# Performance work log

Hardware: AMD Instinct MI355X
Metric: run time of the kernel (lower is better)

The kernel has to match this reference:

```python
import jax, jax.numpy as jnp
import numpy as np

B, S, D = 2, 2048, 768
H, HD = 12, 64
PAST = 2048
MAXPOS = PAST + S  # 4096


def setup_inputs() -> dict:
    key = jax.random.key(0)
    ks = jax.random.split(key, 9)
    hidden_states = jax.random.normal(ks[0], (B, S, D), dtype=jnp.float32)
    layer_past = jax.random.normal(ks[1], (2, B, H, PAST, HD), dtype=jnp.float32)
    # GPT-2 style causal multiplicative mask over full context length
    mask = jnp.tril(jnp.ones((MAXPOS, MAXPOS), dtype=jnp.float32))[None, None, :, :]
    Wq = jax.random.normal(ks[2], (D, D), dtype=jnp.float32) * 0.02
    bq = jnp.zeros((D,), dtype=jnp.float32)
    Wk = jax.random.normal(ks[3], (D, D), dtype=jnp.float32) * 0.02
    bk = jnp.zeros((D,), dtype=jnp.float32)
    Wv = jax.random.normal(ks[4], (D, D), dtype=jnp.float32) * 0.02
    bv = jnp.zeros((D,), dtype=jnp.float32)
    return {"hidden_states": hidden_states, "layer_past": layer_past, "mask": mask,
            "Wq": Wq, "bq": bq, "Wk": Wk, "bk": bk, "Wv": Wv, "bv": bv}


def _split_heads(x):
    b, s, _ = x.shape
    return x.reshape(b, s, H, HD).transpose(0, 2, 1, 3)  # [B,H,S,HD]


def reference(hidden_states, layer_past, mask, Wq, bq, Wk, bk, Wv, bv):
    q = _split_heads(hidden_states @ Wq + bq)
    k = _split_heads(hidden_states @ Wk + bk)
    v = _split_heads(hidden_states @ Wv + bv)
    # KV-cache concat along sequence dim
    k = jnp.concatenate((layer_past[0], k), axis=-2)  # [B,H,ns,HD]
    v = jnp.concatenate((layer_past[1], v), axis=-2)
    present = jnp.stack((k, v), axis=0)
    scores = jnp.einsum('bhqd,bhkd->bhqk', q, k) / 8.0  # 8 = sqrt(64)
    nd, ns = scores.shape[-2], scores.shape[-1]
    m = mask[:, :, ns - nd:ns, :ns]
    scores = scores * m - 1e10 * (1.0 - m)
    probs = jax.nn.softmax(scores, axis=-1)  # dropout is identity at eval
    ctx = jnp.einsum('bhqk,bhkd->bhqd', probs, v)
    ctx = ctx.transpose(0, 2, 1, 3).reshape(hidden_states.shape[0], nd, H * HD)
    return ctx, present
```

## Files before the change

### kernel.cpp

```cpp
#include <hip/hip_runtime.h>


typedef unsigned short u16;
typedef __attribute__((ext_vector_type(8))) short bf16x8;
typedef __attribute__((ext_vector_type(4))) float f32x4;

#define CTXN   3145728
#define CHUNK  262144
#define PCHUNK 131072
#define SHAD_NEED ((size_t)12*1024*1024 + (size_t)2*24*64*4096*2)
#define MFMA(a,b,c) __builtin_amdgcn_mfma_f32_16x16x32_bf16(a,b,c,0,0,0)

__device__ __forceinline__ u16 f2b(float f) {
    union { float f; unsigned int i; } u; u.f = f;
    unsigned int r = u.i + 0x7fffu + ((u.i >> 16) & 1u);
    return (u16)(r >> 16);
}
__device__ __forceinline__ unsigned int pk2(float lo, float hi) {
    unsigned int lr = __float_as_uint(lo); lr += 0x7fffu + ((lr >> 16) & 1u);
    unsigned int hr = __float_as_uint(hi); hr += 0x7fffu + ((hr >> 16) & 1u);
    return __builtin_amdgcn_perm(hr, lr, 0x07060302u);
}
union U8 { unsigned int w[4]; bf16x8 v; };

__device__ __forceinline__ int vpos(int k) {
    return (k & 32) | ((k & 12) << 1) | ((k & 16) >> 2) | (k & 3);
}
__device__ __forceinline__ int vkey(int p) {
    return (p & 32) | ((p & 4) << 2) | ((p & 24) >> 1) | (p & 3);
}

__global__ __launch_bounds__(256) void prep_w(
    const float* __restrict__ Wq, const float* __restrict__ Wk,
    const float* __restrict__ Wv, u16* __restrict__ WT)
{
    __shared__ __align__(16) u16 tile[64][72];
    const float* W = blockIdx.z == 0 ? Wq : (blockIdx.z == 1 ? Wk : Wv);
    const int r0 = blockIdx.y * 64, c0 = blockIdx.x * 64;
    const int t = threadIdx.x;
#pragma unroll
    for (int i = 0; i < 2; i++) {
        int idx = t + 256 * i, r = idx >> 3, c8 = idx & 7;
        const float* src = &W[(size_t)(r0 + r) * 768 + c0 + c8 * 8];
        u16 tmp[8];
#pragma unroll
        for (int j = 0; j < 8; j++) tmp[j] = f2b(src[j]);
        *(uint4*)&tile[r][c8 * 8] = *(uint4*)tmp;
    }
    __syncthreads();
#pragma unroll
    for (int i = 0; i < 2; i++) {
        int idx = t + 256 * i, n = idx >> 3, k8 = idx & 7;
        u16 tmp[8];
#pragma unroll
        for (int j = 0; j < 8; j++) tmp[j] = tile[k8 * 8 + j][n];
        *(uint4*)&WT[((size_t)blockIdx.z * 768 + c0 + n) * 768 + r0 + k8 * 8] = *(uint4*)tmp;
    }
}

__global__ __launch_bounds__(256) void prep_h(const float* __restrict__ Hs,
                                              u16* __restrict__ Hb)
{
    size_t base = ((size_t)blockIdx.x * 256 + threadIdx.x) * 16;
    u16 tmp[16];
#pragma unroll
    for (int j = 0; j < 16; j++) tmp[j] = f2b(Hs[base + j]);
    *(uint4*)&Hb[base] = *(uint4*)tmp;
    *(uint4*)&Hb[base + 8] = *(uint4*)(tmp + 8);
}

__global__ __launch_bounds__(256) void past_prep(const float* __restrict__ past,
                                                 float* __restrict__ out,
                                                 u16* __restrict__ shad)
{
    __shared__ float Vl[64][65];
    const int bh = blockIdx.x, kb = blockIdx.y, t = threadIdx.x;
    const int key = t >> 2, qd = t & 3;
    const float* Ks = past + (size_t)bh * PCHUNK + (size_t)kb * 4096;
    const float* Vs = past + (size_t)(24 + bh) * PCHUNK + (size_t)kb * 4096;
    float* Ko = out + (size_t)CTXN + (size_t)bh * CHUNK + (size_t)kb * 4096;
    float* Vo = out + (size_t)CTXN + (size_t)(24 + bh) * CHUNK + (size_t)kb * 4096;

    float4 kv[4], vv[4];
#pragma unroll
    for (int j = 0; j < 4; j++) {
        kv[j] = *(const float4*)&Ks[key * 64 + qd * 16 + j * 4];
        vv[j] = *(const float4*)&Vs[key * 64 + qd * 16 + j * 4];
    }
#pragma unroll
    for (int j = 0; j < 4; j++) {
        *(float4*)&Ko[key * 64 + qd * 16 + j * 4] = kv[j];
        *(float4*)&Vo[key * 64 + qd * 16 + j * 4] = vv[j];
        *(float4*)&Vl[key][qd * 16 + j * 4] = vv[j];
    }
    if (shad) {
        u16* Ksh = shad + (size_t)(bh * 64 + kb) * 4096;
        const float* kf = (const float*)kv;
        u16 a[8], bb[8];
#pragma unroll
        for (int j = 0; j < 8; j++) { a[j] = f2b(kf[j]); bb[j] = f2b(kf[8 + j]); }
        *(uint4*)&Ksh[key * 64 + (((2 * qd) ^ (key & 7)) * 8)] = *(uint4*)a;
        *(uint4*)&Ksh[key * 64 + (((2 * qd + 1) ^ (key & 7)) * 8)] = *(uint4*)bb;
    }
    __syncthreads();
    if (shad) {
        u16* Vsh = shad + (size_t)(1536 + bh * 64 + kb) * 4096;
        const int d = t & 63, ph = t >> 6;
#pragma unroll
        for (int s2 = 0; s2 < 2; s2++) {
            int sp = ph * 2 + s2;
            u16 c[8];
#pragma unroll
            for (int j = 0; j < 8; j++)
                c[j] = f2b(Vl[vkey(sp * 8 + j)][d]);
            *(uint4*)&Vsh[d * 64 + ((sp ^ (d & 7)) * 8)] = *(uint4*)c;
        }
    }
}

__global__ __launch_bounds__(256) void qkv_gemm(
    const u16* __restrict__ Hb, const u16* __restrict__ WT,
    const float* __restrict__ bq, const float* __restrict__ bk,
    const float* __restrict__ bv, float* out, u16* shad)
{
    __shared__ __align__(16) u16 Al[128][72];
    __shared__ __align__(16) u16 Bl[128][72];
    const int t = threadIdx.x, lane = t & 63, w = t >> 6;
    const int wr = w >> 1, wc = w & 1;
    const int g = lane >> 4, li = lane & 15;
    const int m0 = blockIdx.y * 128, n0 = blockIdx.x * 128;
    f32x4 acc[4][4] = {};

    for (int k0 = 0; k0 < 768; k0 += 64) {
#pragma unroll
        for (int i = 0; i < 4; i++) {
            int idx = t + 256 * i, r = idx >> 3, c8 = idx & 7;
            *(uint4*)&Al[r][c8 * 8] = *(const uint4*)&Hb[(size_t)(m0 + r) * 768 + k0 + c8 * 8];
            *(uint4*)&Bl[r][c8 * 8] = *(const uint4*)&WT[(size_t)(n0 + r) * 768 + k0 + c8 * 8];
        }
        __syncthreads();
#pragma unroll
        for (int kk = 0; kk < 64; kk += 32) {
            bf16x8 af[4], bf[4];
#pragma unroll
            for (int mi = 0; mi < 4; mi++)
                af[mi] = *(const bf16x8*)&Al[wr * 64 + mi * 16 + li][kk + g * 8];
#pragma unroll
            for (int ni = 0; ni < 4; ni++)
                bf[ni] = *(const bf16x8*)&Bl[wc * 64 + ni * 16 + li][kk + g * 8];
#pragma unroll
            for (int mi = 0; mi < 4; mi++)
#pragma unroll
                for (int ni = 0; ni < 4; ni++)
                    acc[mi][ni] = MFMA(af[mi], bf[ni], acc[mi][ni]);
        }
        __syncthreads();
    }

#pragma unroll
    for (int mi = 0; mi < 4; mi++) {
#pragma unroll
        for (int ni = 0; ni < 4; ni++) {
            int col = n0 + wc * 64 + ni * 16 + li;
            int which = col >= 1536 ? 2 : (col >= 768 ? 1 : 0);
            int c2 = col - which * 768;
            int h = c2 >> 6, hd = c2 & 63;
            float bias = which == 0 ? bq[c2] : which == 1 ? bk[c2] : bv[c2];
            int rowb = m0 + wr * 64 + mi * 16 + g * 4;
#pragma unroll
            for (int r = 0; r < 4; r++) {
                int rr = rowb + r;
                float o = acc[mi][ni][r] + bias;
                if (which == 0) {
                    out[(size_t)rr * 768 + c2] = o;
                } else {
                    int b = rr >> 11, s = rr & 2047;
                    size_t off = (size_t)CTXN +
                        ((size_t)((which - 1) * 2 + b) * 12 + h) * CHUNK +
                        (size_t)(2048 + s) * 64 + hd;
                    out[off] = o;
                    if (shad) {
                        int bh2 = b * 12 + h;
                        int keyg = 2048 + s;
                        u16 ob = f2b(o);
                        if (which == 1)
                            shad[((size_t)(bh2 * 64 + (keyg >> 6))) * 4096
                                 + (keyg & 63) * 64 + (((hd >> 3) ^ (keyg & 7)) * 8)
                                 + (hd & 7)] = ob;
                        else {
                            int pos = vpos(keyg & 63);
                            shad[((size_t)(1536 + bh2 * 64 + (keyg >> 6))) * 4096
                                 + hd * 64 + (((pos >> 3) ^ (hd & 7)) * 8)
                                 + (pos & 7)] = ob;
                        }
                    }
                }
            }
        }
    }
}

#define SOFTMAX_RESCALE(S, M, L, O)                                              \
    {                                                                            \
        float tm = fmaxf(fmaxf(S[0][0], S[0][1]), fmaxf(S[0][2], S[0][3]));      \
        _Pragma("unroll")                                                        \
        for (int nt = 1; nt < 8; nt++)                                           \
            tm = fmaxf(tm, fmaxf(fmaxf(S[nt][0], S[nt][1]),                      \
                                 fmaxf(S[nt][2], S[nt][3])));                    \
        tm = fmaxf(tm, __shfl_xor(tm, 16));                                      \
        tm = fmaxf(tm, __shfl_xor(tm, 32));                                      \
        float mn = fmaxf(M, tm);                                                 \
        float al = __builtin_amdgcn_exp2f(M - mn);                               \
        M = mn;                                                                  \
        float ts = 0.f;                                                          \
        _Pragma("unroll")                                                        \
        for (int nt = 0; nt < 8; nt++) {                                         \
            _Pragma("unroll")                                                    \
            for (int r = 0; r < 4; r++) {                                        \
                float p = __builtin_amdgcn_exp2f(S[nt][r] - mn);                 \
                S[nt][r] = p; ts += p;                                           \
            }                                                                    \
        }                                                                        \
        ts += __shfl_xor(ts, 16);                                                \
        ts += __shfl_xor(ts, 32);                                                \
        L = L * al + ts;                                                         \
        float av[4];                                                             \
        _Pragma("unroll")                                                        \
        for (int r = 0; r < 4; r++) av[r] = __shfl(al, (g << 4) + (g << 2) + r); \
        _Pragma("unroll")                                                        \
        for (int dt = 0; dt < 4; dt++) {                                         \
            _Pragma("unroll")                                                    \
            for (int r = 0; r < 4; r++) O[dt][r] *= av[r];                       \
        }                                                                        \
    }

__global__ __launch_bounds__(128, 2) void attn2(const u16* __restrict__ shad, float* out)
{
    __shared__ __align__(16) u16 KV[16384];
    const int bh = blockIdx.x;
    const int qt = 31 - blockIdx.y;
    const int b = bh / 12, h = bh - 12 * b;
    const int t = threadIdx.x, lane = t & 63, w = t >> 6;
    const int g = lane >> 4, li = lane & 15, liq = li & 7;
    char* ldsb = (char*)KV;
    const char* Kp = (const char*)(shad + (size_t)bh * 262144);
    const char* Vp = (const char*)(shad + (size_t)(1536 + bh * 64) * 4096);

    const int qw = qt * 64 + w * 32;
    const float qs = 0.125f * 1.44269504f;
    u16 qa[32];
    const float* QA = out + ((size_t)b * 2048 + qw + li) * 768 + h * 64;
    const float* QB = QA + 16 * 768;
#pragma unroll
    for (int j = 0; j < 8; j++) {
        qa[j]      = f2b(QA[g * 8 + j] * qs);
        qa[8 + j]  = f2b(QA[32 + g * 8 + j] * qs);
        qa[16 + j] = f2b(QB[g * 8 + j] * qs);
        qa[24 + j] = f2b(QB[32 + g * 8 + j] * qs);
    }
    bf16x8 qA0 = *(bf16x8*)qa,        qA1 = *(bf16x8*)(qa + 8);
    bf16x8 qB0 = *(bf16x8*)(qa + 16), qB1 = *(bf16x8*)(qa + 24);

    const int koff0 = (g ^ liq) * 16, koff1 = ((4 + g) ^ liq) * 16;
    int voff[4];
#pragma unroll
    for (int ks = 0; ks < 4; ks++)
        voff[ks] = (ks >> 1) * 8192 + ((((ks & 1) * 4 + g) ^ liq) * 16);

    f32x4 oA[4] = {}, oB[4] = {};
    float mA = -30000.f, lA = 0.f, mB = -30000.f, lB = 0.f;

    const int nk64 = 33 + qt;
    const int nIter = (nk64 + 1) >> 1;
    const int qoff = (qt & 1) ? 64 : 0;

    for (int it = 0; it < nIter; ++it) {
        {
            const char* gK = Kp + (size_t)it * 16384;
            const char* gV = Vp + (size_t)it * 16384;
            const int off0 = w * 1024 + lane * 16;
#pragma unroll
            for (int i = 0; i < 8; i++) {
                int off = i * 2048 + off0;
                __builtin_amdgcn_global_load_lds(
                    (const __attribute__((address_space(1))) unsigned int*)(gK + off),
                    (__attribute__((address_space(3))) unsigned int*)(ldsb + off), 16, 0, 0);
                __builtin_amdgcn_global_load_lds(
                    (const __attribute__((address_space(1))) unsigned int*)(gV + off),
                    (__attribute__((address_space(3))) unsigned int*)(ldsb + 16384 + off), 16, 0, 0);
            }
        }
        __syncthreads();

        f32x4 sA[8], sB[8];
#pragma unroll
        for (int nt = 0; nt < 8; nt++) {
            const char* kr = ldsb + (nt * 16 + li) * 128;
            bf16x8 k0 = *(const bf16x8*)(kr + koff0);
            bf16x8 k1 = *(const bf16x8*)(kr + koff1);
            f32x4 a = {};
            a = MFMA(k0, qA0, a); a = MFMA(k1, qA1, a); sA[nt] = a;
            f32x4 c = {};
            c = MFMA(k0, qB0, c); c = MFMA(k1, qB1, c); sB[nt] = c;
        }
        if (it == nIter - 1) {
#pragma unroll
            for (int nt = 0; nt < 8; nt++)
#pragma unroll
                for (int r = 0; r < 4; r++) {
                    int kl = nt * 16 + 4 * g + r;
                    if (kl > qoff + w * 32 + li)      sA[nt][r] = -30000.f;
                    if (kl > qoff + w * 32 + 16 + li) sB[nt][r] = -30000.f;
                }
        }

        SOFTMAX_RESCALE(sA, mA, lA, oA)
        SOFTMAX_RESCALE(sB, mB, lB, oB)

#pragma unroll
        for (int ks = 0; ks < 4; ks++) {
            U8 pa, pb;
            pa.w[0] = pk2(sA[2 * ks][0],     sA[2 * ks][1]);
            pa.w[1] = pk2(sA[2 * ks][2],     sA[2 * ks][3]);
            pa.w[2] = pk2(sA[2 * ks + 1][0], sA[2 * ks + 1][1]);
            pa.w[3] = pk2(sA[2 * ks + 1][2], sA[2 * ks + 1][3]);
            pb.w[0] = pk2(sB[2 * ks][0],     sB[2 * ks][1]);
            pb.w[1] = pk2(sB[2 * ks][2],     sB[2 * ks][3]);
            pb.w[2] = pk2(sB[2 * ks + 1][0], sB[2 * ks + 1][1]);
            pb.w[3] = pk2(sB[2 * ks + 1][2], sB[2 * ks + 1][3]);
#pragma unroll
            for (int dt = 0; dt < 4; dt++) {
                bf16x8 vf = *(const bf16x8*)(ldsb + 16384 + (dt * 16 + li) * 128 + voff[ks]);
                oA[dt] = MFMA(pa.v, vf, oA[dt]);
                oB[dt] = MFMA(pb.v, vf, oB[dt]);
            }
        }
        __syncthreads();
    }

    float ivA = 1.0f / lA, ivB = 1.0f / lB;
    float iA[4], iB[4];
#pragma unroll
    for (int r = 0; r < 4; r++) {
        iA[r] = __shfl(ivA, (g << 4) + (g << 2) + r);
        iB[r] = __shfl(ivB, (g << 4) + (g << 2) + r);
    }
#pragma unroll
    for (int dt = 0; dt < 4; dt++)
#pragma unroll
        for (int r = 0; r < 4; r++) {
            size_t rowA = (size_t)b * 2048 + qw + 4 * g + r;
            out[rowA * 768 + h * 64 + dt * 16 + li]        = oA[dt][r] * iA[r];
            out[(rowA + 16) * 768 + h * 64 + dt * 16 + li] = oB[dt][r] * iB[r];
        }
}

__global__ __launch_bounds__(256) void attn(float* out)
{
    __shared__ __align__(16) u16 Kl[64][72];
    __shared__ __align__(16) u16 Vt[64][72];
    __shared__ __align__(16) u16 Pl[4][16][72];
    const int bh = blockIdx.x;
    const int qt = 31 - blockIdx.y;
    const int b = bh / 12, h = bh - 12 * b;
    const int t = threadIdx.x, lane = t & 63, w = t >> 6;
    const int g = lane >> 4, li = lane & 15;
    const size_t kbase = (size_t)CTXN + (size_t)bh * CHUNK;
    const size_t vbase = kbase + (size_t)24 * CHUNK;
    const int q0 = qt * 64;

    const float* Qp = out + ((size_t)b * 2048 + q0 + w * 16 + li) * 768 + h * 64;
    u16 qa[16];
#pragma unroll
    for (int j = 0; j < 8; j++) qa[j]     = f2b(Qp[g * 8 + j]);
#pragma unroll
    for (int j = 0; j < 8; j++) qa[8 + j] = f2b(Qp[32 + g * 8 + j]);
    bf16x8 qf0 = *(bf16x8*)qa, qf1 = *(bf16x8*)(qa + 8);

    f32x4 o[4] = {};
    float mrun[4], lsum[4];
#pragma unroll
    for (int r = 0; r < 4; r++) { mrun[r] = -30000.0f; lsum[r] = 0.f; }

    const int nkb = 33 + qt;
    for (int kb = 0; kb < nkb; kb++) {
#pragma unroll
        for (int i = 0; i < 2; i++) {
            int idx = t + 256 * i, r = idx >> 3, c8 = idx & 7;
            const float* src = &out[kbase + (size_t)(kb * 64 + r) * 64 + c8 * 8];
            u16 tmp[8];
#pragma unroll
            for (int j = 0; j < 8; j++) tmp[j] = f2b(src[j]);
            *(uint4*)&Kl[r][c8 * 8] = *(uint4*)tmp;
        }
#pragma unroll
        for (int i = 0; i < 2; i++) {
            int idx = t + 256 * i, d = idx >> 3, k8 = idx & 7;
            u16 tmp[8];
#pragma unroll
            for (int j = 0; j < 8; j++)
                tmp[j] = f2b(out[vbase + (size_t)(kb * 64 + k8 * 8 + j) * 64 + d]);
            *(uint4*)&Vt[d][k8 * 8] = *(uint4*)tmp;
        }
        __syncthreads();

        f32x4 sc[4];
#pragma unroll
        for (int nt = 0; nt < 4; nt++) {
            bf16x8 kf0 = *(const bf16x8*)&Kl[nt * 16 + li][g * 8];
            bf16x8 kf1 = *(const bf16x8*)&Kl[nt * 16 + li][32 + g * 8];
            f32x4 a = {};
            a = MFMA(qf0, kf0, a);
            a = MFMA(qf1, kf1, a);
            sc[nt] = a;
        }
        const bool diag = (kb == nkb - 1);
#pragma unroll
        for (int nt = 0; nt < 4; nt++)
#pragma unroll
            for (int r = 0; r < 4; r++) {
                float s = sc[nt][r] * 0.125f;
                if (diag) {
                    int key_l = nt * 16 + li, q_l = w * 16 + g * 4 + r;
                    if (key_l > q_l) s = -30000.0f;
                }
                sc[nt][r] = s;
            }
        float alpha[4];
#pragma unroll
        for (int r = 0; r < 4; r++) {
            float tm = fmaxf(fmaxf(sc[0][r], sc[1][r]), fmaxf(sc[2][r], sc[3][r]));
#pragma unroll
            for (int off = 1; off < 16; off <<= 1) tm = fmaxf(tm, __shfl_xor(tm, off));
            float mn = fmaxf(mrun[r], tm);
            alpha[r] = __expf(mrun[r] - mn);
            mrun[r] = mn;
            float ts = 0.f;
#pragma unroll
            for (int nt = 0; nt < 4; nt++) {
                float p = __expf(sc[nt][r] - mn);
                sc[nt][r] = p;
                ts += p;
            }
#pragma unroll
            for (int off = 1; off < 16; off <<= 1) ts += __shfl_xor(ts, off);
            lsum[r] = lsum[r] * alpha[r] + ts;
        }
#pragma unroll
        for (int dt = 0; dt < 4; dt++)
#pragma unroll
            for (int r = 0; r < 4; r++) o[dt][r] *= alpha[r];

#pragma unroll
        for (int nt = 0; nt < 4; nt++)
#pragma unroll
            for (int r = 0; r < 4; r++)
                Pl[w][g * 4 + r][nt * 16 + li] = f2b(sc[nt][r]);

        bf16x8 pa0 = *(const bf16x8*)&Pl[w][li][g * 8];
        bf16x8 pa1 = *(const bf16x8*)&Pl[w][li][32 + g * 8];
#pragma unroll
        for (int dt = 0; dt < 4; dt++) {
            bf16x8 vf0 = *(const bf16x8*)&Vt[dt * 16 + li][g * 8];
            bf16x8 vf1 = *(const bf16x8*)&Vt[dt * 16 + li][32 + g * 8];
            o[dt] = MFMA(pa0, vf0, o[dt]);
            o[dt] = MFMA(pa1, vf1, o[dt]);
        }
        __syncthreads();
    }

    float inv[4];
#pragma unroll
    for (int r = 0; r < 4; r++) inv[r] = 1.0f / lsum[r];
#pragma unroll
    for (int dt = 0; dt < 4; dt++)
#pragma unroll
        for (int r = 0; r < 4; r++) {
            int q = q0 + w * 16 + g * 4 + r;
            out[((size_t)b * 2048 + q) * 768 + h * 64 + dt * 16 + li] = o[dt][r] * inv[r];
        }
}

extern "C" void kernel_launch(void* const* d_in, const int* in_sizes, int n_in,
                              void* d_out, int out_size, void* d_ws, size_t ws_size,
                              hipStream_t stream) {
    (void)in_sizes; (void)n_in; (void)out_size;
    const float* Hs   = (const float*)d_in[0];
    const float* past = (const float*)d_in[1];
    const float* Wq = (const float*)d_in[3];
    const float* bq = (const float*)d_in[4];
    const float* Wk = (const float*)d_in[5];
    const float* bk = (const float*)d_in[6];
    const float* Wv = (const float*)d_in[7];
    const float* bv = (const float*)d_in[8];
    float* out = (float*)d_out;
    u16* WT   = (u16*)d_ws;
    u16* Hb   = (u16*)((char*)d_ws + (4  << 20));
    u16* shad = (u16*)((char*)d_ws + (12 << 20));
    const bool useShadow = ws_size >= SHAD_NEED;

    prep_w<<<dim3(12, 12, 3), 256, 0, stream>>>(Wq, Wk, Wv, WT);
    prep_h<<<dim3(768), 256, 0, stream>>>(Hs, Hb);
    past_prep<<<dim3(24, 32), 256, 0, stream>>>(past, out,
                                                useShadow ? shad : (u16*)nullptr);
    qkv_gemm<<<dim3(18, 32), 256, 0, stream>>>(Hb, WT, bq, bk, bv, out,
                                               useShadow ? shad : (u16*)nullptr);
    if (useShadow)
        attn2<<<dim3(24, 32), 128, 0, stream>>>(shad, out);
    else
        attn<<<dim3(24, 32), 256, 0, stream>>>(out);
}
```

Baseline: 300.1 us.

## Double-buffer attention K/V tiles, widen query tile, move shadow writes to separate kernel

```diff
diff --git a/kernel.cpp b/kernel.cpp
--- a/kernel.cpp
+++ b/kernel.cpp
@@ -118,10 +118,53 @@
     }
 }
 
+__global__ __launch_bounds__(256) void shadow_new(const float* __restrict__ out,
+                                                  u16* __restrict__ shad)
+{
+    __shared__ float Vl[64][65];
+    const int bh = blockIdx.x, kb = blockIdx.y, t = threadIdx.x;
+    const int key = t >> 2, qd = t & 3;
+    const float* Ks = out + (size_t)CTXN + (size_t)bh * CHUNK + (size_t)(2048 + kb * 64) * 64;
+    const float* Vs = out + (size_t)CTXN + (size_t)(24 + bh) * CHUNK + (size_t)(2048 + kb * 64) * 64;
+
+    float4 kv[4], vv[4];
+#pragma unroll
+    for (int j = 0; j < 4; j++) {
+        kv[j] = *(const float4*)&Ks[key * 64 + qd * 16 + j * 4];
+        vv[j] = *(const float4*)&Vs[key * 64 + qd * 16 + j * 4];
+    }
+#pragma unroll
+    for (int j = 0; j < 4; j++)
+        *(float4*)&Vl[key][qd * 16 + j * 4] = vv[j];
+    {
+        u16* Ksh = shad + (size_t)(bh * 64 + 32 + kb) * 4096;
+        const float* kf = (const float*)kv;
+        u16 a[8], bb[8];
+#pragma unroll
+        for (int j = 0; j < 8; j++) { a[j] = f2b(kf[j]); bb[j] = f2b(kf[8 + j]); }
+        *(uint4*)&Ksh[key * 64 + (((2 * qd) ^ (key & 7)) * 8)] = *(uint4*)a;
+        *(uint4*)&Ksh[key * 64 + (((2 * qd + 1) ^ (key & 7)) * 8)] = *(uint4*)bb;
+    }
+    __syncthreads();
+    {
+        u16* Vsh = shad + (size_t)(1536 + bh * 64 + 32 + kb) * 4096;
+        const int d = t & 63, ph = t >> 6;
+#pragma unroll
+        for (int s2 = 0; s2 < 2; s2++) {
+            int sp = ph * 2 + s2;
+            u16 c[8];
+#pragma unroll
+            for (int j = 0; j < 8; j++)
+                c[j] = f2b(Vl[vkey(sp * 8 + j)][d]);
+            *(uint4*)&Vsh[d * 64 + ((sp ^ (d & 7)) * 8)] = *(uint4*)c;
+        }
+    }
+}
+
 __global__ __launch_bounds__(256) void qkv_gemm(
     const u16* __restrict__ Hb, const u16* __restrict__ WT,
     const float* __restrict__ bq, const float* __restrict__ bk,
-    const float* __restrict__ bv, float* out, u16* shad)
+    const float* __restrict__ bv, float* out)
 {
     __shared__ __align__(16) u16 Al[128][72];
     __shared__ __align__(16) u16 Bl[128][72];
@@ -179,21 +222,6 @@
                         ((size_t)((which - 1) * 2 + b) * 12 + h) * CHUNK +
                         (size_t)(2048 + s) * 64 + hd;
                     out[off] = o;
-                    if (shad) {
-                        int bh2 = b * 12 + h;
-                        int keyg = 2048 + s;
-                        u16 ob = f2b(o);
-                        if (which == 1)
-                            shad[((size_t)(bh2 * 64 + (keyg >> 6))) * 4096
-                                 + (keyg & 63) * 64 + (((hd >> 3) ^ (keyg & 7)) * 8)
-                                 + (hd & 7)] = ob;
-                        else {
-                            int pos = vpos(keyg & 63);
-                            shad[((size_t)(1536 + bh2 * 64 + (keyg >> 6))) * 4096
-                                 + hd * 64 + (((pos >> 3) ^ (hd & 7)) * 8)
-                                 + (pos & 7)] = ob;
-                        }
-                    }
                 }
             }
         }
@@ -234,11 +262,30 @@
         }                                                                        \
     }
 
-__global__ __launch_bounds__(128, 2) void attn2(const u16* __restrict__ shad, float* out)
-{
-    __shared__ __align__(16) u16 KV[16384];
+#define STAGE(buf_, it_)                                                                   \
+    {                                                                                      \
+        const char* gK_ = Kp + (size_t)(it_) * 16384;                                      \
+        const char* gV_ = Vp + (size_t)(it_) * 16384;                                      \
+        char* lds_ = ldsb + (buf_) * 32768;                                                \
+        const int o_ = t * 16;                                                             \
+        _Pragma("unroll")                                                                  \
+        for (int i_ = 0; i_ < 4; i_++) {                                                   \
+            __builtin_amdgcn_global_load_lds(                                              \
+                (const __attribute__((address_space(1))) unsigned int*)(gK_ + o_ + i_ * 4096), \
+                (__attribute__((address_space(3))) unsigned int*)(lds_ + o_ + i_ * 4096),  \
+                16, 0, 0);                                                                 \
+            __builtin_amdgcn_global_load_lds(                                              \
+                (const __attribute__((address_space(1))) unsigned int*)(gV_ + o_ + i_ * 4096), \
+                (__attribute__((address_space(3))) unsigned int*)(lds_ + 16384 + o_ + i_ * 4096), \
+                16, 0, 0);                                                                 \
+        }                                                                                  \
+    }
+
+__global__ __launch_bounds__(256, 2) void attn2(const u16* __restrict__ shad, float* out)
+{
+    __shared__ __align__(16) u16 KV[32768];
     const int bh = blockIdx.x;
-    const int qt = 31 - blockIdx.y;
+    const int qt = 15 - blockIdx.y;
     const int b = bh / 12, h = bh - 12 * b;
     const int t = threadIdx.x, lane = t & 63, w = t >> 6;
     const int g = lane >> 4, li = lane & 15, liq = li & 7;
@@ -246,7 +293,7 @@
     const char* Kp = (const char*)(shad + (size_t)bh * 262144);
     const char* Vp = (const char*)(shad + (size_t)(1536 + bh * 64) * 4096);
 
-    const int qw = qt * 64 + w * 32;
+    const int qw = qt * 128 + w * 32;
     const float qs = 0.125f * 1.44269504f;
     u16 qa[32];
     const float* QA = out + ((size_t)b * 2048 + qw + li) * 768 + h * 64;
@@ -270,32 +317,22 @@
     f32x4 oA[4] = {}, oB[4] = {};
     float mA = -30000.f, lA = 0.f, mB = -30000.f, lB = 0.f;
 
-    const int nk64 = 33 + qt;
-    const int nIter = (nk64 + 1) >> 1;
-    const int qoff = (qt & 1) ? 64 : 0;
+    const int nIter = 17 + qt;
+
+    STAGE(0, 0)
+    __syncthreads();
 
     for (int it = 0; it < nIter; ++it) {
-        {
-            const char* gK = Kp + (size_t)it * 16384;
-            const char* gV = Vp + (size_t)it * 16384;
-            const int off0 = w * 1024 + lane * 16;
-#pragma unroll
-            for (int i = 0; i < 8; i++) {
-                int off = i * 2048 + off0;
-                __builtin_amdgcn_global_load_lds(
-                    (const __attribute__((address_space(1))) unsigned int*)(gK + off),
-                    (__attribute__((address_space(3))) unsigned int*)(ldsb + off), 16, 0, 0);
-                __builtin_amdgcn_global_load_lds(
-                    (const __attribute__((address_space(1))) unsigned int*)(gV + off),
-                    (__attribute__((address_space(3))) unsigned int*)(ldsb + 16384 + off), 16, 0, 0);
-            }
-        }
-        __syncthreads();
+        const int buf = it & 1;
+        if (it + 1 < nIter) STAGE(buf ^ 1, it + 1)
+
+        const char* lK = ldsb + buf * 32768;
+        const char* lV = lK + 16384;
 
         f32x4 sA[8], sB[8];
 #pragma unroll
         for (int nt = 0; nt < 8; nt++) {
-            const char* kr = ldsb + (nt * 16 + li) * 128;
+            const char* kr = lK + (nt * 16 + li) * 128;
             bf16x8 k0 = *(const bf16x8*)(kr + koff0);
             bf16x8 k1 = *(const bf16x8*)(kr + koff1);
             f32x4 a = {};
@@ -309,8 +346,8 @@
 #pragma unroll
                 for (int r = 0; r < 4; r++) {
                     int kl = nt * 16 + 4 * g + r;
-                    if (kl > qoff + w * 32 + li)      sA[nt][r] = -30000.f;
-                    if (kl > qoff + w * 32 + 16 + li) sB[nt][r] = -30000.f;
+                    if (kl > w * 32 + li)      sA[nt][r] = -30000.f;
+                    if (kl > w * 32 + 16 + li) sB[nt][r] = -30000.f;
                 }
         }
 
@@ -330,7 +367,7 @@
             pb.w[3] = pk2(sB[2 * ks + 1][2], sB[2 * ks + 1][3]);
 #pragma unroll
             for (int dt = 0; dt < 4; dt++) {
-                bf16x8 vf = *(const bf16x8*)(ldsb + 16384 + (dt * 16 + li) * 128 + voff[ks]);
+                bf16x8 vf = *(const bf16x8*)(lV + (dt * 16 + li) * 128 + voff[ks]);
                 oA[dt] = MFMA(pa.v, vf, oA[dt]);
                 oB[dt] = MFMA(pb.v, vf, oB[dt]);
             }
@@ -503,10 +540,11 @@
     prep_h<<<dim3(768), 256, 0, stream>>>(Hs, Hb);
     past_prep<<<dim3(24, 32), 256, 0, stream>>>(past, out,
                                                 useShadow ? shad : (u16*)nullptr);
-    qkv_gemm<<<dim3(18, 32), 256, 0, stream>>>(Hb, WT, bq, bk, bv, out,
-                                               useShadow ? shad : (u16*)nullptr);
-    if (useShadow)
-        attn2<<<dim3(24, 32), 128, 0, stream>>>(shad, out);
-    else
+    qkv_gemm<<<dim3(18, 32), 256, 0, stream>>>(Hb, WT, bq, bk, bv, out);
+    if (useShadow) {
+        shadow_new<<<dim3(24, 32), 256, 0, stream>>>(out, shad);
+        attn2<<<dim3(24, 16), 256, 0, stream>>>(shad, out);
+    } else {
         attn<<<dim3(24, 32), 256, 0, stream>>>(out);
-}
+    }
+}
```

Result: faster. 289.6 us (-3.5%).
